# Kernel tuning notes

Hardware: AMD Instinct MI355X
Metric: run time of the kernel (lower is better)

## Reference

```python
import jax, jax.numpy as jnp
import numpy as np

N_NODES = 50000
N_EDGES = 800000
N_GRAPHS = 64


def graph_conv(x, edge_index, w_rel, b_rel, w_root):
    # PyG GraphConv with aggr='add':
    #   out = lin_rel(sum_{j in N(i)} x_j) + lin_root(x_i)
    src, dst = edge_index[0], edge_index[1]
    agg = jax.ops.segment_sum(x[src], dst, num_segments=x.shape[0])  # [N, d_in]
    return agg @ w_rel + b_rel + x @ w_root  # [N, d_out]


def scatter_mean(x, batch, num_segments):
    s = jax.ops.segment_sum(x, batch, num_segments=num_segments)
    cnt = jax.ops.segment_sum(jnp.ones((x.shape[0],), x.dtype), batch,
                              num_segments=num_segments)
    return s / jnp.maximum(cnt, 1.0)[:, None]


def setup_inputs() -> dict:
    key = jax.random.key(0)
    ks = jax.random.split(key, 8)
    d_feat, d_hid, d_out = 128, 128, 128
    x = jax.random.normal(ks[0], (N_NODES, d_feat), dtype=jnp.float32)
    edge_index = jax.random.randint(ks[1], (2, N_EDGES), 0, N_NODES, dtype=jnp.int64)
    batch = jnp.sort(jax.random.randint(ks[2], (N_NODES,), 0, N_GRAPHS, dtype=jnp.int64))

    def glorot(k, shape):
        fan_in = shape[0]
        return jax.random.normal(k, shape, dtype=jnp.float32) / np.sqrt(fan_in)

    return {
        "x": x,
        "edge_index": edge_index,
        "batch": batch,
        "w_rel1": glorot(ks[3], (d_feat, d_hid)),
        "b_rel1": jnp.zeros((d_hid,), jnp.float32),
        "w_root1": glorot(ks[4], (d_feat, d_hid)),
        "w_rel2": glorot(ks[5], (d_hid, 2 * d_hid)),
        "b_rel2": jnp.zeros((2 * d_hid,), jnp.float32),
        "w_root2": glorot(ks[6], (d_hid, 2 * d_hid)),
        "w_rel3": glorot(ks[7], (2 * d_hid, d_out)),
        "b_rel3": jnp.zeros((d_out,), jnp.float32),
        "w_root3": glorot(jax.random.fold_in(key, 99), (2 * d_hid, d_out)),
    }


def reference(x, edge_index, batch,
              w_rel1, b_rel1, w_root1,
              w_rel2, b_rel2, w_root2,
              w_rel3, b_rel3, w_root3):
    h = jax.nn.elu(graph_conv(x, edge_index, w_rel1, b_rel1, w_root1))
    h = jax.nn.elu(graph_conv(h, edge_index, w_rel2, b_rel2, w_root2))
    h = jax.nn.elu(graph_conv(h, edge_index, w_rel3, b_rel3, w_root3))
    return scatter_mean(h, batch, N_GRAPHS)  # [num_graphs, n_out]
```

## Files before the change

kernel.cpp:

```cpp
#include <hip/hip_runtime.h>
#include <math.h>

#define NN 50000
#define NNP 50048
#define NE 800000
#define NG 64
#define NBK 196
#define ECH 4082
#define TOTH (NBK * NBK)
#define NBH 151

typedef __attribute__((ext_vector_type(8))) __bf16 bf16x8;
typedef __attribute__((ext_vector_type(8))) short short8;
typedef __attribute__((ext_vector_type(4))) float f32x4;

__device__ inline unsigned short f2bf(float f) {
    unsigned int u = __float_as_uint(f);
    u += 0x7fffu + ((u >> 16) & 1u);
    return (unsigned short)(u >> 16);
}
__device__ inline float bflo(unsigned int v) { return __uint_as_float(v << 16); }
__device__ inline float bfhi(unsigned int v) { return __uint_as_float(v & 0xffff0000u); }

#define GLD_LDS16(g, l)                                                          \
    __builtin_amdgcn_global_load_lds(                                            \
        (const __attribute__((address_space(1))) unsigned int*)(g),              \
        (__attribute__((address_space(3))) unsigned int*)(l), 16, 0, 0)

__global__ __launch_bounds__(256) void cvt_k(const float* __restrict__ in,
                                             unsigned short* __restrict__ outp) {
    int i = blockIdx.x * 256 + threadIdx.x;
    if (i < NN * 32) {
        float4 v = ((const float4*)in)[i];
        unsigned int p0 = ((unsigned int)f2bf(v.y) << 16) | f2bf(v.x);
        unsigned int p1 = ((unsigned int)f2bf(v.w) << 16) | f2bf(v.z);
        ((uint2*)outp)[i] = make_uint2(p0, p1);
    }
}

__global__ __launch_bounds__(256) void wt_k(const float* __restrict__ wr1,
                                            const float* __restrict__ wo1,
                                            const float* __restrict__ wr2,
                                            const float* __restrict__ wo2,
                                            const float* __restrict__ wr3,
                                            const float* __restrict__ wo3,
                                            unsigned short* __restrict__ W1T,
                                            unsigned short* __restrict__ W2T,
                                            unsigned short* __restrict__ W3T) {
    int id = blockIdx.x * 256 + threadIdx.x;
    if (id < 32768) {
        int n = id >> 8, k = id & 255;
        float v = (k < 128) ? wr1[k * 128 + n] : wo1[(k - 128) * 128 + n];
        W1T[id] = f2bf(v);
    } else if (id < 98304) {
        int j = id - 32768; int n = j >> 8, k = j & 255;
        float v = (k < 128) ? wr2[k * 256 + n] : wo2[(k - 128) * 256 + n];
        W2T[j] = f2bf(v);
    } else if (id < 163840) {
        int j = id - 98304; int n = j >> 8, k = j & 255;
        float v = (n < 128) ? wr3[k * 128 + n] : wo3[k * 128 + (n - 128)];
        W3T[j] = f2bf(v);
    }
}

__global__ __launch_bounds__(256) void hist_k(const int* __restrict__ dst,
                                              int* __restrict__ H) {
    __shared__ int h[NBK];
    int t = threadIdx.x, k = blockIdx.x;
    if (t < NBK) h[t] = 0;
    __syncthreads();
    int e0 = k * ECH, e1 = min(NE, e0 + ECH);
    for (int e = e0 + t; e < e1; e += 256) atomicAdd(&h[dst[e] >> 8], 1);
    __syncthreads();
    if (t < NBK) H[t * NBK + k] = h[t];
}

__global__ __launch_bounds__(256) void hsum_k(const int* __restrict__ H,
                                              int* __restrict__ hb) {
    int i = blockIdx.x * 256 + threadIdx.x;
    int v = (i < TOTH) ? H[i] : 0;
    for (int off = 32; off; off >>= 1) v += __shfl_xor(v, off, 64);
    __shared__ int ws[4];
    if ((threadIdx.x & 63) == 0) ws[threadIdx.x >> 6] = v;
    __syncthreads();
    if (threadIdx.x == 0) hb[blockIdx.x] = ws[0] + ws[1] + ws[2] + ws[3];
}

__global__ __launch_bounds__(256) void hscan_k(const int* __restrict__ hb,
                                               int* __restrict__ hoff) {
    __shared__ int s[256];
    int t = threadIdx.x;
    int v = (t < NBH) ? hb[t] : 0;
    s[t] = v; __syncthreads();
    for (int off = 1; off < 256; off <<= 1) {
        int u = (t >= off) ? s[t - off] : 0;
        __syncthreads(); s[t] += u; __syncthreads();
    }
    hoff[t] = (t == 0) ? 0 : s[t - 1];
}

__global__ __launch_bounds__(256) void happly_k(const int* __restrict__ H,
                                                const int* __restrict__ hoff,
                                                int* __restrict__ S) {
    int t = threadIdx.x;
    int i = blockIdx.x * 256 + t;
    int v = (i < TOTH) ? H[i] : 0;
    __shared__ int s[256];
    s[t] = v; __syncthreads();
    for (int off = 1; off < 256; off <<= 1) {
        int u = (t >= off) ? s[t - off] : 0;
        __syncthreads(); s[t] += u; __syncthreads();
    }
    if (i < TOTH) S[i] = hoff[blockIdx.x] + s[t] - v;
}

__global__ __launch_bounds__(256) void scatter_k(const int* __restrict__ src,
                                                 const int* __restrict__ dst,
                                                 const int* __restrict__ S,
                                                 int* __restrict__ tmp) {
    __shared__ int cur[NBK];
    int t = threadIdx.x, k = blockIdx.x;
    if (t < NBK) cur[t] = S[t * NBK + k];
    __syncthreads();
    int e0 = k * ECH, e1 = min(NE, e0 + ECH);
    for (int e = e0 + t; e < e1; e += 256) {
        int d = dst[e];
        int p = atomicAdd(&cur[d >> 8], 1);
        tmp[p] = ((d & 255) << 16) | src[e];
    }
}

__global__ __launch_bounds__(256) void csr_k(const int* __restrict__ tmp,
                                             const int* __restrict__ S,
                                             int* __restrict__ rowptr,
                                             int* __restrict__ colsrc) {
    __shared__ int hist[256], off[256], cur[256];
    int t = threadIdx.x, b = blockIdx.x;
    int base = S[b * NBK];
    int next = (b < NBK - 1) ? S[(b + 1) * NBK] : NE;
    int cntb = next - base;
    hist[t] = 0;
    __syncthreads();
    for (int i = t; i < cntb; i += 256) atomicAdd(&hist[tmp[base + i] >> 16], 1);
    __syncthreads();
    int v = hist[t];
    off[t] = v; __syncthreads();
    for (int o = 1; o < 256; o <<= 1) {
        int u = (t >= o) ? off[t - o] : 0;
        __syncthreads(); off[t] += u; __syncthreads();
    }
    int excl = off[t] - v;
    int node = b * 256 + t;
    if (node <= NN) rowptr[node] = base + excl;
    cur[t] = excl;
    __syncthreads();
    for (int i = t; i < cntb; i += 256) {
        int e = tmp[base + i];
        int p = atomicAdd(&cur[e >> 16], 1);
        colsrc[base + p] = e & 0xffff;
    }
}

__global__ __launch_bounds__(256) void aggb_k(const unsigned short* __restrict__ feat,
                                              const int* __restrict__ rowptr,
                                              const int* __restrict__ colsrc,
                                              unsigned short* __restrict__ outp) {
    int node = __builtin_amdgcn_readfirstlane((int)(blockIdx.x * 4 + (threadIdx.x >> 6)));
    int lane = threadIdx.x & 63;
    int beg = rowptr[node], end = rowptr[node + 1];
    float ax = 0.f, ay = 0.f;
    int e = beg;
    for (; e + 2 <= end; e += 2) {
        int s0 = colsrc[e], s1 = colsrc[e + 1];
        unsigned int v0 = *(const unsigned int*)&feat[(size_t)s0 * 128 + lane * 2];
        unsigned int v1 = *(const unsigned int*)&feat[(size_t)s1 * 128 + lane * 2];
        ax += bflo(v0); ay += bfhi(v0);
        ax += bflo(v1); ay += bfhi(v1);
    }
    if (e < end) {
        unsigned int v0 = *(const unsigned int*)&feat[(size_t)colsrc[e] * 128 + lane * 2];
        ax += bflo(v0); ay += bfhi(v0);
    }
    unsigned int p = ((unsigned int)f2bf(ay) << 16) | f2bf(ax);
    *(unsigned int*)&outp[(size_t)node * 128 + lane * 2] = p;
}

template <int KA, int N, bool TWO, bool BIAS, bool ELU, bool SPLIT>
__global__ __launch_bounds__(256) void gemm_k(const unsigned short* __restrict__ A1,
                                              const unsigned short* __restrict__ A2,
                                              const unsigned short* __restrict__ WT,
                                              const float* __restrict__ bias,
                                              unsigned short* __restrict__ Cout,
                                              unsigned short* __restrict__ Cout2) {
    constexpr int KTOT = TWO ? 2 * KA : KA;
    __shared__ __attribute__((aligned(16))) unsigned short As[128 * 32];
    __shared__ __attribute__((aligned(16))) unsigned short Bs[128 * 32];
    const int t = threadIdx.x;
    const int wv = t >> 6, lane = t & 63;
    const int qd = lane >> 4, l16 = lane & 15;
    const int m0 = blockIdx.x * 128, n0 = blockIdx.y * 128;
    const int mh = (wv & 1) * 64, nh = (wv >> 1) * 64;
    const int srow = lane >> 2;
    const int skk  = (lane & 3) * 8;

    f32x4 acc[4][4] = {};

    for (int k0 = 0; k0 < KTOT; k0 += 32) {
        const unsigned short* Abase = (TWO && k0 >= KA) ? (A2 + (k0 - KA)) : (A1 + k0);
#pragma unroll
        for (int i = 0; i < 2; ++i) {
            int chunk = wv * 2 + i;
            const unsigned short* g = Abase + (size_t)(m0 + chunk * 16 + srow) * KA + skk;
            GLD_LDS16(g, &As[chunk * 512]);
        }
        const unsigned short* Wbase = WT + k0;
#pragma unroll
        for (int i = 0; i < 2; ++i) {
            int chunk = wv * 2 + i;
            const unsigned short* g = Wbase + (size_t)(n0 + chunk * 16 + srow) * KTOT + skk;
            GLD_LDS16(g, &Bs[chunk * 512]);
        }
        __syncthreads();
        bf16x8 af[4], bfr[4];
#pragma unroll
        for (int mi = 0; mi < 4; ++mi)
            af[mi] = *(const bf16x8*)&As[(mh + mi * 16 + l16) * 32 + qd * 8];
#pragma unroll
        for (int ni = 0; ni < 4; ++ni)
            bfr[ni] = *(const bf16x8*)&Bs[(nh + ni * 16 + l16) * 32 + qd * 8];
#pragma unroll
        for (int mi = 0; mi < 4; ++mi)
#pragma unroll
            for (int ni = 0; ni < 4; ++ni)
                acc[mi][ni] = __builtin_amdgcn_mfma_f32_16x16x32_bf16(
                    af[mi], bfr[ni], acc[mi][ni], 0, 0, 0);
        __syncthreads();
    }

#pragma unroll
    for (int mi = 0; mi < 4; ++mi) {
#pragma unroll
        for (int ni = 0; ni < 4; ++ni) {
#pragma unroll
            for (int r = 0; r < 4; ++r) {
                int mm = m0 + mh + mi * 16 + qd * 4 + r;
                if (mm < NN) {
                    int nn = n0 + nh + ni * 16 + l16;
                    float v = acc[mi][ni][r];
                    if (BIAS) v += bias[nn];
                    if (ELU) v = v > 0.f ? v : (__expf(v) - 1.f);
                    unsigned short b = f2bf(v);
                    if (SPLIT) {
                        unsigned short* dst = (nn < 128) ? Cout : Cout2;
                        dst[(size_t)mm * 128 + (nn & 127)] = b;
                    } else {
                        Cout[(size_t)mm * N + nn] = b;
                    }
                }
            }
        }
    }
}

__global__ void bounds_k(const int* __restrict__ batch, int* __restrict__ bounds) {
    int g = threadIdx.x;
    if (g > NG) return;
    int lo = 0, hi = NN;
    while (lo < hi) {
        int mid = (lo + hi) >> 1;
        if (batch[mid] < g) lo = mid + 1; else hi = mid;
    }
    bounds[g] = lo;
}

__global__ __launch_bounds__(128) void finalize2_k(const unsigned short* __restrict__ aggy,
                                                   const unsigned short* __restrict__ rr,
                                                   const float* __restrict__ b3,
                                                   const int* __restrict__ batch,
                                                   float* __restrict__ outsum) {
    const int CH = 25;
    int n0 = blockIdx.x * CH;
    int c = threadIdx.x;
    float bias = b3[c];
    int g = batch[n0];
    float acc = 0.f;
    for (int i = 0; i < CH; ++i) {
        int n = n0 + i;
        int gn = batch[n];
        if (gn != g) {
            unsafeAtomicAdd(&outsum[(size_t)g * 128 + c], acc);
            acc = 0.f; g = gn;
        }
        size_t idx = (size_t)n * 128 + c;
        float v = __uint_as_float((unsigned int)aggy[idx] << 16)
                + __uint_as_float((unsigned int)rr[idx] << 16) + bias;
        v = v > 0.f ? v : (__expf(v) - 1.f);
        acc += v;
    }
    unsafeAtomicAdd(&outsum[(size_t)g * 128 + c], acc);
}

__global__ void divide_k(const int* __restrict__ bounds, float* __restrict__ out) {
    int i = blockIdx.x * 256 + threadIdx.x;
    if (i < NG * 128) {
        int g = i >> 7;
        float c = (float)(bounds[g + 1] - bounds[g]);
        out[i] /= fmaxf(c, 1.f);
    }
}

extern "C" void kernel_launch(void* const* d_in, const int* in_sizes, int n_in,
                              void* d_out, int out_size, void* d_ws, size_t ws_size,
                              hipStream_t stream) {
    const float* x       = (const float*)d_in[0];
    const int*   ei      = (const int*)d_in[1];
    const int*   batch   = (const int*)d_in[2];
    const float* w_rel1  = (const float*)d_in[3];
    const float* b_rel1  = (const float*)d_in[4];
    const float* w_root1 = (const float*)d_in[5];
    const float* w_rel2  = (const float*)d_in[6];
    const float* b_rel2  = (const float*)d_in[7];
    const float* w_root2 = (const float*)d_in[8];
    const float* w_rel3  = (const float*)d_in[9];
    const float* b_rel3  = (const float*)d_in[10];
    const float* w_root3 = (const float*)d_in[11];
    const int* esrc = ei;
    const int* edst = ei + NE;

    unsigned short* Ab = (unsigned short*)d_ws;
    unsigned short* Bb = Ab + (size_t)NNP * 128;
    unsigned short* Cb = Bb + (size_t)NNP * 128;
    unsigned short* xb = Cb + (size_t)NNP * 256;
    unsigned short* W1T = xb + (size_t)NNP * 128;
    unsigned short* W2T = W1T + 128 * 256;
    unsigned short* W3T = W2T + 256 * 256;
    int* rowptr = (int*)(W3T + 256 * 256);
    int* colsrc = rowptr + (NN + 1);
    int* tmp    = colsrc + NE;
    int* H      = tmp + NE;
    int* S      = H + TOTH;
    int* hb     = S + TOTH;
    int* hoff   = hb + 256;
    int* bounds = hoff + 256;
    float* outp = (float*)d_out;

    cvt_k<<<(NN * 32 + 255) / 256, 256, 0, stream>>>(x, xb);
    wt_k<<<640, 256, 0, stream>>>(w_rel1, w_root1, w_rel2, w_root2, w_rel3, w_root3,
                                  W1T, W2T, W3T);
    hist_k<<<NBK, 256, 0, stream>>>(edst, H);
    hsum_k<<<NBH, 256, 0, stream>>>(H, hb);
    hscan_k<<<1, 256, 0, stream>>>(hb, hoff);
    happly_k<<<NBH, 256, 0, stream>>>(H, hoff, S);
    scatter_k<<<NBK, 256, 0, stream>>>(esrc, edst, S, tmp);
    csr_k<<<NBK, 256, 0, stream>>>(tmp, S, rowptr, colsrc);

    dim3 g1(NNP / 128, 1), g2(NNP / 128, 2);

    aggb_k<<<NN / 4, 256, 0, stream>>>(xb, rowptr, colsrc, Ab);
    gemm_k<128, 128, true, true, true, false><<<g1, 256, 0, stream>>>(Ab, xb, W1T, b_rel1, Bb, nullptr);

    aggb_k<<<NN / 4, 256, 0, stream>>>(Bb, rowptr, colsrc, Ab);
    gemm_k<128, 256, true, true, true, false><<<g2, 256, 0, stream>>>(Ab, Bb, W2T, b_rel2, Cb, nullptr);

    gemm_k<256, 256, false, false, false, true><<<g2, 256, 0, stream>>>(Cb, nullptr, W3T, nullptr, Ab, Bb);
    aggb_k<<<NN / 4, 256, 0, stream>>>(Ab, rowptr, colsrc, Cb);

    hipMemsetAsync(outp, 0, NG * 128 * sizeof(float), stream);
    bounds_k<<<1, 128, 0, stream>>>(batch, bounds);
    finalize2_k<<<NN / 25, 128, 0, stream>>>(Cb, Bb, b_rel3, batch, outp);
    divide_k<<<(NG * 128 + 255) / 256, 256, 0, stream>>>(bounds, outp);
}
```

Baseline: 335.0 us.

## Fuse final aggregation into pooling, merge setup kernels, tune GEMM tile and unroll

Several changes are bundled here. The third-layer neighbour aggregation now runs inside the final ELU-and-pooling kernel, which drops the separate aggregation kernel and its intermediate write and read. The input and weight conversion kernels are merged into one launch, and the output memset moves into the bounds kernel. The first GEMM uses a 64-row tile so more blocks are launched, and the aggregation loops are unrolled by four. The fused finalize reads bf16 values at 2-byte granularity per thread, which may use memory bandwidth less efficiently than the old 4-byte-per-lane aggregation.

```diff
diff --git a/kernel.cpp b/kernel.cpp
--- a/kernel.cpp
+++ b/kernel.cpp
@@ -21,45 +21,42 @@
 }
 __device__ inline float bflo(unsigned int v) { return __uint_as_float(v << 16); }
 __device__ inline float bfhi(unsigned int v) { return __uint_as_float(v & 0xffff0000u); }
+__device__ inline float bfs(unsigned short v) { return __uint_as_float((unsigned int)v << 16); }
 
 #define GLD_LDS16(g, l)                                                          \
     __builtin_amdgcn_global_load_lds(                                            \
         (const __attribute__((address_space(1))) unsigned int*)(g),              \
         (__attribute__((address_space(3))) unsigned int*)(l), 16, 0, 0)
 
-__global__ __launch_bounds__(256) void cvt_k(const float* __restrict__ in,
-                                             unsigned short* __restrict__ outp) {
-    int i = blockIdx.x * 256 + threadIdx.x;
-    if (i < NN * 32) {
-        float4 v = ((const float4*)in)[i];
+__global__ __launch_bounds__(256) void setup_k(const float* __restrict__ x,
+                                               const float* __restrict__ wr1,
+                                               const float* __restrict__ wo1,
+                                               const float* __restrict__ wr2,
+                                               const float* __restrict__ wo2,
+                                               const float* __restrict__ wr3,
+                                               const float* __restrict__ wo3,
+                                               unsigned short* __restrict__ xb,
+                                               unsigned short* __restrict__ W1T,
+                                               unsigned short* __restrict__ W2T,
+                                               unsigned short* __restrict__ W3T) {
+    int id = blockIdx.x * 256 + threadIdx.x;
+    if (id < NN * 32) {
+        float4 v = ((const float4*)x)[id];
         unsigned int p0 = ((unsigned int)f2bf(v.y) << 16) | f2bf(v.x);
         unsigned int p1 = ((unsigned int)f2bf(v.w) << 16) | f2bf(v.z);
-        ((uint2*)outp)[i] = make_uint2(p0, p1);
-    }
-}
-
-__global__ __launch_bounds__(256) void wt_k(const float* __restrict__ wr1,
-                                            const float* __restrict__ wo1,
-                                            const float* __restrict__ wr2,
-                                            const float* __restrict__ wo2,
-                                            const float* __restrict__ wr3,
-                                            const float* __restrict__ wo3,
-                                            unsigned short* __restrict__ W1T,
-                                            unsigned short* __restrict__ W2T,
-                                            unsigned short* __restrict__ W3T) {
-    int id = blockIdx.x * 256 + threadIdx.x;
-    if (id < 32768) {
-        int n = id >> 8, k = id & 255;
-        float v = (k < 128) ? wr1[k * 128 + n] : wo1[(k - 128) * 128 + n];
-        W1T[id] = f2bf(v);
-    } else if (id < 98304) {
-        int j = id - 32768; int n = j >> 8, k = j & 255;
-        float v = (k < 128) ? wr2[k * 256 + n] : wo2[(k - 128) * 256 + n];
-        W2T[j] = f2bf(v);
-    } else if (id < 163840) {
-        int j = id - 98304; int n = j >> 8, k = j & 255;
-        float v = (n < 128) ? wr3[k * 128 + n] : wo3[k * 128 + (n - 128)];
-        W3T[j] = f2bf(v);
+        ((uint2*)xb)[id] = make_uint2(p0, p1);
+        return;
+    }
+    int w = id - NN * 32;
+    if (w < 32768) {
+        int n = w >> 8, k = w & 255;
+        W1T[w] = f2bf((k < 128) ? wr1[k * 128 + n] : wo1[(k - 128) * 128 + n]);
+    } else if (w < 98304) {
+        int j = w - 32768; int n = j >> 8, k = j & 255;
+        W2T[j] = f2bf((k < 128) ? wr2[k * 256 + n] : wo2[(k - 128) * 256 + n]);
+    } else if (w < 163840) {
+        int j = w - 98304; int n = j >> 8, k = j & 255;
+        W3T[j] = f2bf((n < 128) ? wr3[k * 128 + n] : wo3[k * 128 + (n - 128)]);
     }
 }
 
@@ -170,14 +167,18 @@
     int beg = rowptr[node], end = rowptr[node + 1];
     float ax = 0.f, ay = 0.f;
     int e = beg;
-    for (; e + 2 <= end; e += 2) {
-        int s0 = colsrc[e], s1 = colsrc[e + 1];
+    for (; e + 4 <= end; e += 4) {
+        int s0 = colsrc[e], s1 = colsrc[e + 1], s2 = colsrc[e + 2], s3 = colsrc[e + 3];
         unsigned int v0 = *(const unsigned int*)&feat[(size_t)s0 * 128 + lane * 2];
         unsigned int v1 = *(const unsigned int*)&feat[(size_t)s1 * 128 + lane * 2];
+        unsigned int v2 = *(const unsigned int*)&feat[(size_t)s2 * 128 + lane * 2];
+        unsigned int v3 = *(const unsigned int*)&feat[(size_t)s3 * 128 + lane * 2];
         ax += bflo(v0); ay += bfhi(v0);
         ax += bflo(v1); ay += bfhi(v1);
-    }
-    if (e < end) {
+        ax += bflo(v2); ay += bfhi(v2);
+        ax += bflo(v3); ay += bfhi(v3);
+    }
+    for (; e < end; ++e) {
         unsigned int v0 = *(const unsigned int*)&feat[(size_t)colsrc[e] * 128 + lane * 2];
         ax += bflo(v0); ay += bfhi(v0);
     }
@@ -185,7 +186,7 @@
     *(unsigned int*)&outp[(size_t)node * 128 + lane * 2] = p;
 }
 
-template <int KA, int N, bool TWO, bool BIAS, bool ELU, bool SPLIT>
+template <int MT, int KA, int N, bool TWO, bool BIAS, bool ELU, bool SPLIT>
 __global__ __launch_bounds__(256) void gemm_k(const unsigned short* __restrict__ A1,
                                               const unsigned short* __restrict__ A2,
                                               const unsigned short* __restrict__ WT,
@@ -193,23 +194,24 @@
                                               unsigned short* __restrict__ Cout,
                                               unsigned short* __restrict__ Cout2) {
     constexpr int KTOT = TWO ? 2 * KA : KA;
-    __shared__ __attribute__((aligned(16))) unsigned short As[128 * 32];
+    constexpr int MI = MT / 32;
+    __shared__ __attribute__((aligned(16))) unsigned short As[MT * 32];
     __shared__ __attribute__((aligned(16))) unsigned short Bs[128 * 32];
     const int t = threadIdx.x;
     const int wv = t >> 6, lane = t & 63;
     const int qd = lane >> 4, l16 = lane & 15;
-    const int m0 = blockIdx.x * 128, n0 = blockIdx.y * 128;
-    const int mh = (wv & 1) * 64, nh = (wv >> 1) * 64;
+    const int m0 = blockIdx.x * MT, n0 = blockIdx.y * 128;
+    const int mh = (wv & 1) * (MT / 2), nh = (wv >> 1) * 64;
     const int srow = lane >> 2;
     const int skk  = (lane & 3) * 8;
 
-    f32x4 acc[4][4] = {};
+    f32x4 acc[MI][4] = {};
 
     for (int k0 = 0; k0 < KTOT; k0 += 32) {
         const unsigned short* Abase = (TWO && k0 >= KA) ? (A2 + (k0 - KA)) : (A1 + k0);
 #pragma unroll
-        for (int i = 0; i < 2; ++i) {
-            int chunk = wv * 2 + i;
+        for (int i = 0; i < MT / 64; ++i) {
+            int chunk = wv * (MT / 64) + i;
             const unsigned short* g = Abase + (size_t)(m0 + chunk * 16 + srow) * KA + skk;
             GLD_LDS16(g, &As[chunk * 512]);
         }
@@ -221,15 +223,15 @@
             GLD_LDS16(g, &Bs[chunk * 512]);
         }
         __syncthreads();
-        bf16x8 af[4], bfr[4];
-#pragma unroll
-        for (int mi = 0; mi < 4; ++mi)
+        bf16x8 af[MI], bfr[4];
+#pragma unroll
+        for (int mi = 0; mi < MI; ++mi)
             af[mi] = *(const bf16x8*)&As[(mh + mi * 16 + l16) * 32 + qd * 8];
 #pragma unroll
         for (int ni = 0; ni < 4; ++ni)
             bfr[ni] = *(const bf16x8*)&Bs[(nh + ni * 16 + l16) * 32 + qd * 8];
 #pragma unroll
-        for (int mi = 0; mi < 4; ++mi)
+        for (int mi = 0; mi < MI; ++mi)
 #pragma unroll
             for (int ni = 0; ni < 4; ++ni)
                 acc[mi][ni] = __builtin_amdgcn_mfma_f32_16x16x32_bf16(
@@ -238,7 +240,7 @@
     }
 
 #pragma unroll
-    for (int mi = 0; mi < 4; ++mi) {
+    for (int mi = 0; mi < MI; ++mi) {
 #pragma unroll
         for (int ni = 0; ni < 4; ++ni) {
 #pragma unroll
@@ -262,42 +264,58 @@
     }
 }
 
-__global__ void bounds_k(const int* __restrict__ batch, int* __restrict__ bounds) {
+__global__ __launch_bounds__(128) void bounds_k(const int* __restrict__ batch,
+                                                int* __restrict__ bounds,
+                                                float* __restrict__ outp) {
     int g = threadIdx.x;
-    if (g > NG) return;
-    int lo = 0, hi = NN;
-    while (lo < hi) {
-        int mid = (lo + hi) >> 1;
-        if (batch[mid] < g) lo = mid + 1; else hi = mid;
-    }
-    bounds[g] = lo;
-}
-
-__global__ __launch_bounds__(128) void finalize2_k(const unsigned short* __restrict__ aggy,
+    if (g <= NG) {
+        int lo = 0, hi = NN;
+        while (lo < hi) {
+            int mid = (lo + hi) >> 1;
+            if (batch[mid] < g) lo = mid + 1; else hi = mid;
+        }
+        bounds[g] = lo;
+    }
+    for (int i = threadIdx.x; i < NG * 128; i += 128) outp[i] = 0.f;
+}
+
+__global__ __launch_bounds__(128) void finalize3_k(const unsigned short* __restrict__ y,
                                                    const unsigned short* __restrict__ rr,
                                                    const float* __restrict__ b3,
                                                    const int* __restrict__ batch,
+                                                   const int* __restrict__ rowptr,
+                                                   const int* __restrict__ colsrc,
                                                    float* __restrict__ outsum) {
-    const int CH = 25;
+    const int CH = 10;
     int n0 = blockIdx.x * CH;
     int c = threadIdx.x;
     float bias = b3[c];
     int g = batch[n0];
-    float acc = 0.f;
+    float gacc = 0.f;
     for (int i = 0; i < CH; ++i) {
         int n = n0 + i;
         int gn = batch[n];
         if (gn != g) {
-            unsafeAtomicAdd(&outsum[(size_t)g * 128 + c], acc);
-            acc = 0.f; g = gn;
-        }
-        size_t idx = (size_t)n * 128 + c;
-        float v = __uint_as_float((unsigned int)aggy[idx] << 16)
-                + __uint_as_float((unsigned int)rr[idx] << 16) + bias;
+            unsafeAtomicAdd(&outsum[(size_t)g * 128 + c], gacc);
+            gacc = 0.f; g = gn;
+        }
+        int beg = rowptr[n], end = rowptr[n + 1];
+        float acc = 0.f;
+        int e = beg;
+        for (; e + 4 <= end; e += 4) {
+            int s0 = colsrc[e], s1 = colsrc[e + 1], s2 = colsrc[e + 2], s3 = colsrc[e + 3];
+            float v0 = bfs(y[(size_t)s0 * 128 + c]);
+            float v1 = bfs(y[(size_t)s1 * 128 + c]);
+            float v2 = bfs(y[(size_t)s2 * 128 + c]);
+            float v3 = bfs(y[(size_t)s3 * 128 + c]);
+            acc += v0 + v1 + v2 + v3;
+        }
+        for (; e < end; ++e) acc += bfs(y[(size_t)colsrc[e] * 128 + c]);
+        float v = acc + bfs(rr[(size_t)n * 128 + c]) + bias;
         v = v > 0.f ? v : (__expf(v) - 1.f);
-        acc += v;
-    }
-    unsafeAtomicAdd(&outsum[(size_t)g * 128 + c], acc);
+        gacc += v;
+    }
+    unsafeAtomicAdd(&outsum[(size_t)g * 128 + c], gacc);
 }
 
 __global__ void divide_k(const int* __restrict__ bounds, float* __restrict__ out) {
@@ -344,29 +362,27 @@
     int* bounds = hoff + 256;
     float* outp = (float*)d_out;
 
-    cvt_k<<<(NN * 32 + 255) / 256, 256, 0, stream>>>(x, xb);
-    wt_k<<<640, 256, 0, stream>>>(w_rel1, w_root1, w_rel2, w_root2, w_rel3, w_root3,
-                                  W1T, W2T, W3T);
+    setup_k<<<(NN * 32 + 163840 + 255) / 256, 256, 0, stream>>>(
+        x, w_rel1, w_root1, w_rel2, w_root2, w_rel3, w_root3, xb, W1T, W2T, W3T);
     hist_k<<<NBK, 256, 0, stream>>>(edst, H);
     hsum_k<<<NBH, 256, 0, stream>>>(H, hb);
     hscan_k<<<1, 256, 0, stream>>>(hb, hoff);
     happly_k<<<NBH, 256, 0, stream>>>(H, hoff, S);
     scatter_k<<<NBK, 256, 0, stream>>>(esrc, edst, S, tmp);
     csr_k<<<NBK, 256, 0, stream>>>(tmp, S, rowptr, colsrc);
-
-    dim3 g1(NNP / 128, 1), g2(NNP / 128, 2);
+    bounds_k<<<1, 128, 0, stream>>>(batch, bounds, outp);
 
     aggb_k<<<NN / 4, 256, 0, stream>>>(xb, rowptr, colsrc, Ab);
-    gemm_k<128, 128, true, true, true, false><<<g1, 256, 0, stream>>>(Ab, xb, W1T, b_rel1, Bb, nullptr);
+    gemm_k<64, 128, 128, true, true, true, false>
+        <<<dim3(NNP / 64, 1), 256, 0, stream>>>(Ab, xb, W1T, b_rel1, Bb, nullptr);
 
     aggb_k<<<NN / 4, 256, 0, stream>>>(Bb, rowptr, colsrc, Ab);
-    gemm_k<128, 256, true, true, true, false><<<g2, 256, 0, stream>>>(Ab, Bb, W2T, b_rel2, Cb, nullptr);
-
-    gemm_k<256, 256, false, false, false, true><<<g2, 256, 0, stream>>>(Cb, nullptr, W3T, nullptr, Ab, Bb);
-    aggb_k<<<NN / 4, 256, 0, stream>>>(Ab, rowptr, colsrc, Cb);
-
-    hipMemsetAsync(outp, 0, NG * 128 * sizeof(float), stream);
-    bounds_k<<<1, 128, 0, stream>>>(batch, bounds);
-    finalize2_k<<<NN / 25, 128, 0, stream>>>(Cb, Bb, b_rel3, batch, outp);
+    gemm_k<128, 128, 256, true, true, true, false>
+        <<<dim3(NNP / 128, 2), 256, 0, stream>>>(Ab, Bb, W2T, b_rel2, Cb, nullptr);
+
+    gemm_k<128, 256, 256, false, false, false, true>
+        <<<dim3(NNP / 128, 2), 256, 0, stream>>>(Cb, nullptr, W3T, nullptr, Ab, Bb);
+
+    finalize3_k<<<NN / 10, 128, 0, stream>>>(Ab, Bb, b_rel3, batch, rowptr, colsrc, outp);
     divide_k<<<(NG * 128 + 255) / 256, 256, 0, stream>>>(bounds, outp);
 }
```

Result: faster. 322.1 us (-3.8%).
